# Performance work log

Measured on AMD Instinct MI355X. Metric: run time of the kernel, lower is better.

Reference implementation:

```python
import jax, jax.numpy as jnp
import numpy as np

DIM = 128
HEADS = 4
KV_RANK = 64
Q_RANK = 32
ROPE = DIM // 2   # 64
NOPE = DIM // 2   # 64
VDIM = DIM // 2   # 64
B, H, W = 2, 64, 64
EPS = 1e-5


def _conv1x1(x, w, b):
    # x: [B,C,H,W], w: [O,C], b: [O]
    return jnp.einsum('bchw,oc->bohw', x, w) + b[None, :, None, None]


def _gn1(x, g, b):
    # GroupNorm with 1 group: normalize over (C,H,W) per sample
    mu = jnp.mean(x, axis=(1, 2, 3), keepdims=True)
    var = jnp.mean((x - mu) ** 2, axis=(1, 2, 3), keepdims=True)
    return (x - mu) / jnp.sqrt(var + EPS) * g[None, :, None, None] + b[None, :, None, None]


def _freqs(h, w):
    # Replicates RotaryPositionalEncoding: pe[...,0::4]=sin_h, 1::4=cos_h, 2::4=sin_w, 3::4=cos_w
    n = ROPE // 4
    inv = 1.0 / (10000.0 ** (jnp.arange(n, dtype=jnp.float32) / n))
    ah = jnp.arange(h, dtype=jnp.float32)[:, None] * inv  # [h,n]
    aw = jnp.arange(w, dtype=jnp.float32)[:, None] * inv  # [w,n]
    fh = jnp.stack([jnp.sin(ah), jnp.cos(ah)], -1)  # [h,n,2] -> (real=sin_h, imag=cos_h)
    fw = jnp.stack([jnp.sin(aw), jnp.cos(aw)], -1)  # [w,n,2]
    fh_b = jnp.broadcast_to(fh[:, None], (h, w, n, 2))
    fw_b = jnp.broadcast_to(fw[None, :], (h, w, n, 2))
    # interleave pairs: pair 2m -> fh[m], pair 2m+1 -> fw[m]
    pe = jnp.stack([fh_b, fw_b], axis=3).reshape(h * w, ROPE // 2, 2)
    return pe  # [S, ROPE//2, 2]


def _rope(x, f):
    # x: [..., S, ROPE]; f: [S, ROPE//2, 2]
    xp = x.reshape(x.shape[:-1] + (ROPE // 2, 2))
    fr, fi = f[..., 0], f[..., 1]  # [S, ROPE//2] broadcast over leading dims
    rr = xp[..., 0] * fr - xp[..., 1] * fi
    ri = xp[..., 0] * fi + xp[..., 1] * fr
    return jnp.stack([rr, ri], -1).reshape(x.shape)


def setup_inputs() -> dict:
    key = jax.random.key(0)
    ks = jax.random.split(key, 8)
    s = 0.02
    inp = {
        'x': jax.random.normal(ks[0], (B, DIM, H, W), dtype=jnp.float32),
        'q1_w': jax.random.normal(ks[1], (Q_RANK, DIM), dtype=jnp.float32) * s,
        'q1_b': jnp.zeros((Q_RANK,), jnp.float32),
        'q_gn_g': jnp.ones((Q_RANK,), jnp.float32),
        'q_gn_b': jnp.zeros((Q_RANK,), jnp.float32),
        'q2_w': jax.random.normal(ks[2], (HEADS * (NOPE + ROPE), Q_RANK), dtype=jnp.float32) * s,
        'q2_b': jnp.zeros((HEADS * (NOPE + ROPE),), jnp.float32),
        'kv1_w': jax.random.normal(ks[3], (KV_RANK + ROPE, DIM), dtype=jnp.float32) * s,
        'kv1_b': jnp.zeros((KV_RANK + ROPE,), jnp.float32),
        'kv_gn_g': jnp.ones((KV_RANK + ROPE,), jnp.float32),
        'kv_gn_b': jnp.zeros((KV_RANK + ROPE,), jnp.float32),
        'kvn_g': jnp.ones((KV_RANK,), jnp.float32),
        'kvn_b': jnp.zeros((KV_RANK,), jnp.float32),
        'kvup_w': jax.random.normal(ks[4], (HEADS * (NOPE + VDIM), KV_RANK), dtype=jnp.float32) * s,
        'kvup_b': jnp.zeros((HEADS * (NOPE + VDIM),), jnp.float32),
        'out_w': jax.random.normal(ks[5], (DIM, HEADS * VDIM), dtype=jnp.float32) * s,
        'out_b': jnp.zeros((DIM,), jnp.float32),
    }
    return inp


def reference(x, q1_w, q1_b, q_gn_g, q_gn_b, q2_w, q2_b, kv1_w, kv1_b, kv_gn_g, kv_gn_b, kvn_g, kvn_b, kvup_w, kvup_b, out_w, out_b):
    b, c, h, w = x.shape
    s = h * w
    f = _freqs(h, w)  # [S, ROPE//2, 2]

    # Q path: low-rank down -> GN -> up
    q = _conv1x1(_gn1(_conv1x1(x, q1_w, q1_b), q_gn_g, q_gn_b), q2_w, q2_b)
    q = q.reshape(b, HEADS, NOPE + ROPE, s).transpose(0, 1, 3, 2)  # [B,H,S,D]
    q_nope, q_rope = q[..., :NOPE], q[..., NOPE:]
    q = jnp.concatenate([q_nope, _rope(q_rope, f)], axis=-1)

    # KV path: joint down-proj, split rope-k and compressed kv
    kv = _gn1(_conv1x1(x, kv1_w, kv1_b), kv_gn_g, kv_gn_b)  # [B, ROPE+KV_RANK, H, W]
    k_rope_c, kv_c = kv[:, :ROPE], kv[:, ROPE:]
    kv_u = _conv1x1(_gn1(kv_c, kvn_g, kvn_b), kvup_w, kvup_b)
    kv_u = kv_u.reshape(b, HEADS, NOPE + VDIM, s).transpose(0, 1, 3, 2)
    k_nope, v = kv_u[..., :NOPE], kv_u[..., NOPE:]

    k_rope = _rope(k_rope_c.reshape(b, ROPE, s).transpose(0, 2, 1)[:, None], f)  # [B,1,S,ROPE]
    k = jnp.concatenate([k_nope, jnp.broadcast_to(k_rope, (b, HEADS, s, ROPE))], axis=-1)

    scale = (NOPE + ROPE) ** -0.5
    attn = jax.nn.softmax(jnp.einsum('bhqd,bhkd->bhqk', q, k) * scale, axis=-1)
    o = jnp.einsum('bhqk,bhkd->bhqd', attn, v)  # [B,H,S,VDIM]
    o = o.transpose(0, 1, 3, 2).reshape(b, HEADS * VDIM, h, w)
    return _conv1x1(o, out_w, out_b) + x
```

## Files before the change

kernel.cpp:

```cpp
#include <hip/hip_runtime.h>

typedef unsigned short ushort_t;
typedef unsigned int uint_t;
typedef __attribute__((ext_vector_type(8))) short s16x8;
typedef __attribute__((ext_vector_type(4))) short s16x4;
typedef __attribute__((ext_vector_type(4))) float f32x4;
typedef __attribute__((ext_vector_type(16))) float f32x16;

#define S_TOT 4096
#define QSCALE 0.08838834764831845f
#define LOG2E 1.4426950408889634f
#define QSL (QSCALE * LOG2E)
#define L2_10000_D16 0.8304820237218406f

__device__ __forceinline__ ushort_t f2b(float f) {
  uint_t u = __float_as_uint(f);
  uint_t r = (u + 0x7FFFu + ((u >> 16) & 1u)) >> 16;
  return (ushort_t)r;
}

__device__ __forceinline__ float b2f(ushort_t u) {
  return __uint_as_float((uint_t)u << 16);
}

__device__ __forceinline__ uint_t cvt_pk_bf16(float lo, float hi) {
  uint_t r;
  asm("v_cvt_pk_bf16_f32 %0, %1, %2" : "=v"(r) : "v"(lo), "v"(hi));
  return r;
}

__device__ __forceinline__ void gload16(const void* g, void* l) {
  __builtin_amdgcn_global_load_lds(
      (const __attribute__((address_space(1))) unsigned int*)g,
      (__attribute__((address_space(3))) unsigned int*)l, 16, 0, 0);
}

__device__ __forceinline__ void rope_pair(float& x0, float& x1, int p, int hi, int wi, float scale) {
  float inv = exp2f(-(float)(p >> 1) * L2_10000_D16);
  float ang = ((p & 1) ? (float)wi : (float)hi) * inv;
  float sn = sinf(ang), cs = cosf(ang);
  float r0 = (x0 * sn - x1 * cs) * scale;
  float r1 = (x0 * cs + x1 * sn) * scale;
  x0 = r0; x1 = r1;
}

__global__ __launch_bounds__(256) void k_conv1(
    const float* __restrict__ x, const float* __restrict__ q1_w, const float* __restrict__ q1_b,
    const float* __restrict__ kv1_w, const float* __restrict__ kv1_b,
    float* __restrict__ y_q, float* __restrict__ y_kv, double* __restrict__ pch,
    const float* __restrict__ q2_w, const float* __restrict__ q2_b,
    const float* __restrict__ kvup_w, const float* __restrict__ kvup_b,
    const float* __restrict__ out_w, const float* __restrict__ out_b,
    ushort_t* __restrict__ wq2, ushort_t* __restrict__ wout,
    float* __restrict__ q2b2, float* __restrict__ outb2) {
  if (blockIdx.x >= 512) {
    int E = (blockIdx.x - 512) * 256 + threadIdx.x;
    if (E < 16384) {
      int oc = E >> 5, r = E & 31;
      int h = oc >> 7, d = oc & 127;
      float val;
      if (d < 64) {
        val = 0.f;
        for (int dd = 0; dd < 64; dd++)
          val += kvup_w[(h * 128 + dd) * 64 + d] * q2_w[(size_t)(h * 128 + dd) * 32 + r];
      } else {
        val = q2_w[(size_t)oc * 32 + r];
      }
      wq2[(size_t)oc * 32 + r] = f2b(val);
    } else if (E < 49152) {
      int e = E - 16384;
      int c = e >> 8, col = e & 255;
      int h = col >> 6, l = col & 63;
      float val = 0.f;
      for (int vd = 0; vd < 64; vd++)
        val += out_w[(size_t)c * 256 + h * 64 + vd] * kvup_w[(h * 128 + 64 + vd) * 64 + l];
      wout[(size_t)c * 256 + col] = f2b(val);
    } else if (E < 49664) {
      int oc = E - 49152;
      int h = oc >> 7, d = oc & 127;
      float val;
      if (d < 64) {
        val = 0.f;
        for (int dd = 0; dd < 64; dd++)
          val += kvup_w[(h * 128 + dd) * 64 + d] * q2_b[h * 128 + dd];
      } else val = q2_b[oc];
      q2b2[oc] = val;
    } else if (E < 49792) {
      int c = E - 49664;
      float val = out_b[c];
      for (int j = 0; j < 256; j++) {
        int h = j >> 6, vd = j & 63;
        val += out_w[(size_t)c * 256 + j] * kvup_b[h * 128 + 64 + vd];
      }
      outb2[c] = val;
    }
    return;
  }
  const int b = blockIdx.x >> 8, blk = blockIdx.x & 255, st = blk * 16;
  const int t = threadIdx.x, si = t & 15, g = t >> 4;
  __shared__ float xs[128][16];
#pragma unroll
  for (int i = 0; i < 8; i++) {
    int c = g + 16 * i;
    xs[c][si] = x[(size_t)(b * 128 + c) * S_TOT + st + si];
  }
  __syncthreads();
  float acc[10];
#pragma unroll
  for (int i = 0; i < 10; i++) {
    int oc = g * 10 + i;
    acc[i] = (oc < 32) ? q1_b[oc] : kv1_b[oc - 32];
  }
  const float4* q1w4 = (const float4*)q1_w;
  const float4* kv1w4 = (const float4*)kv1_w;
  for (int c4 = 0; c4 < 32; c4++) {
    float x0 = xs[c4 * 4 + 0][si], x1 = xs[c4 * 4 + 1][si];
    float x2 = xs[c4 * 4 + 2][si], x3 = xs[c4 * 4 + 3][si];
#pragma unroll
    for (int i = 0; i < 10; i++) {
      int oc = g * 10 + i;
      float4 wv = (oc < 32) ? q1w4[oc * 32 + c4] : kv1w4[(oc - 32) * 32 + c4];
      acc[i] += wv.x * x0 + wv.y * x1 + wv.z * x2 + wv.w * x3;
    }
  }
#pragma unroll
  for (int i = 0; i < 10; i++) {
    int oc = g * 10 + i;
    float a = acc[i];
    if (oc < 32) y_q[(size_t)(b * 32 + oc) * S_TOT + st + si] = a;
    else         y_kv[(size_t)(b * 128 + oc - 32) * S_TOT + st + si] = a;
    double s = a, q = (double)a * a;
#pragma unroll
    for (int o = 1; o < 16; o <<= 1) { s += __shfl_xor(s, o, 16); q += __shfl_xor(q, o, 16); }
    if (si == 0) {
      double* pt = pch + (size_t)(b * 160 + oc) * 512 + blk * 2;
      pt[0] = s; pt[1] = q;
    }
  }
}

__global__ __launch_bounds__(256) void k_red(
    const double* __restrict__ pch, double* __restrict__ SQ) {
  const int pair = blockIdx.x, tid = threadIdx.x;
  const int lane = tid & 63, wid = tid >> 6;
  const double* p = pch + (size_t)pair * 512;
  double s = p[tid * 2], q = p[tid * 2 + 1];
#pragma unroll
  for (int o = 1; o < 64; o <<= 1) { s += __shfl_xor(s, o, 64); q += __shfl_xor(q, o, 64); }
  __shared__ double red[4][2];
  if (lane == 0) { red[wid][0] = s; red[wid][1] = q; }
  __syncthreads();
  if (tid == 0) {
    SQ[pair * 2]     = red[0][0] + red[1][0] + red[2][0] + red[3][0];
    SQ[pair * 2 + 1] = red[0][1] + red[1][1] + red[2][1] + red[3][1];
  }
}

__global__ __launch_bounds__(512) void k_stats(
    const double* __restrict__ SQ,
    const float* __restrict__ qg, const float* __restrict__ qb,
    const float* __restrict__ kvg, const float* __restrict__ kvb,
    const float* __restrict__ kng, const float* __restrict__ knb,
    float* __restrict__ coef) {
  __shared__ double Sh[2][160], Qh[2][160];
  const int tid = threadIdx.x;
  if (tid < 320) {
    int b = tid / 160, c = tid % 160;
    Sh[b][c] = SQ[tid * 2]; Qh[b][c] = SQ[tid * 2 + 1];
  }
  __syncthreads();
  if (tid < 2) {
    int b = tid;
    float* cf = coef + b * 320;
    const double NS = 4096.0;
    double muq = 0, m2q = 0;
    for (int c = 0; c < 32; c++) { muq += Sh[b][c]; m2q += Qh[b][c]; }
    muq /= (32.0 * NS); m2q /= (32.0 * NS);
    double rstdq = 1.0 / sqrt(m2q - muq * muq + 1e-5);
    for (int c = 0; c < 32; c++) {
      double A = rstdq * (double)qg[c];
      cf[c] = (float)A; cf[32 + c] = (float)((double)qb[c] - muq * A);
    }
    double mukv = 0, m2kv = 0;
    for (int c = 0; c < 128; c++) { mukv += Sh[b][32 + c]; m2kv += Qh[b][32 + c]; }
    mukv /= (128.0 * NS); m2kv /= (128.0 * NS);
    double rstdkv = 1.0 / sqrt(m2kv - mukv * mukv + 1e-5);
    for (int c = 0; c < 64; c++) {
      double A = rstdkv * (double)kvg[c];
      cf[64 + c] = (float)A; cf[128 + c] = (float)((double)kvb[c] - mukv * A);
    }
    double mu2 = 0, m22 = 0;
    for (int c2 = 0; c2 < 64; c2++) {
      int c = 64 + c2;
      double a = rstdkv * (double)kvg[c], bb = (double)kvb[c] - mukv * a;
      double Ec = Sh[b][32 + c] / NS, M2c = Qh[b][32 + c] / NS;
      mu2 += a * Ec + bb;
      m22 += a * a * M2c + 2.0 * a * bb * Ec + bb * bb;
    }
    mu2 /= 64.0; m22 /= 64.0;
    double rstd2 = 1.0 / sqrt(m22 - mu2 * mu2 + 1e-5);
    for (int c2 = 0; c2 < 64; c2++) {
      int c = 64 + c2;
      double a = rstdkv * (double)kvg[c], bb = (double)kvb[c] - mukv * a;
      cf[192 + c2] = (float)(a * rstd2 * (double)kng[c2]);
      cf[256 + c2] = (float)((bb - mu2) * rstd2 * (double)kng[c2] + (double)knb[c2]);
    }
  }
}

__global__ __launch_bounds__(256) void k_gq(
    const float* __restrict__ y_q, const float* __restrict__ coef,
    const ushort_t* __restrict__ wq2, const float* __restrict__ q2b2,
    ushort_t* __restrict__ Q) {
  const int id = blockIdx.x;
  const int h = id & 3, st = (id >> 2) & 63, b = id >> 8;
  const int t = threadIdx.x, si = t & 63, wid = t >> 6;
  const int l15 = t & 15, lg = (t >> 4) & 3;
  const float* cf = coef + b * 320;
  __shared__ __align__(16) ushort_t Xt[64][64];
  __shared__ __align__(16) ushort_t sQ[64][128];
  {
    ushort_t pk[8];
#pragma unroll
    for (int j = 0; j < 8; j++) {
      int c = wid * 8 + j;
      float v = y_q[(size_t)(b * 32 + c) * S_TOT + st * 64 + si];
      pk[j] = f2b(v * cf[c] + cf[32 + c]);
    }
    *(s16x8*)((char*)&Xt[si][0] + ((wid * 16) ^ ((si & 7) << 4))) = *(s16x8*)pk;
  }
  __syncthreads();
  const int d0w = wid * 32;
  f32x4 acc[2][4];
#pragma unroll
  for (int db = 0; db < 2; db++) {
    f32x4 bv;
#pragma unroll
    for (int r = 0; r < 4; r++) bv[r] = q2b2[h * 128 + d0w + db * 16 + lg * 4 + r];
#pragma unroll
    for (int sb = 0; sb < 4; sb++) acc[db][sb] = bv;
  }
  s16x8 wf[2];
#pragma unroll
  for (int db = 0; db < 2; db++)
    wf[db] = *(const s16x8*)(wq2 + (size_t)(h * 128 + d0w + db * 16 + l15) * 32 + lg * 8);
  const int xsw = (lg * 16) ^ ((l15 & 7) << 4);
#pragma unroll
  for (int sb = 0; sb < 4; sb++) {
    s16x8 xf = *(const s16x8*)((const char*)&Xt[sb * 16 + l15][0] + xsw);
#pragma unroll
    for (int db = 0; db < 2; db++)
      acc[db][sb] = __builtin_amdgcn_mfma_f32_16x16x32_bf16(wf[db], xf, acc[db][sb], 0, 0, 0);
  }
  if (wid >= 2) {
#pragma unroll
    for (int db = 0; db < 2; db++)
#pragma unroll
      for (int sb = 0; sb < 4; sb++) {
        int sp = st * 64 + sb * 16 + l15, hi = sp >> 6, wi = sp & 63;
        int dg = d0w + db * 16 + lg * 4;
#pragma unroll
        for (int pr = 0; pr < 2; pr++) {
          float v0 = acc[db][sb][pr * 2], v1 = acc[db][sb][pr * 2 + 1];
          int p = (dg + pr * 2 - 64) >> 1;
          rope_pair(v0, v1, p, hi, wi, QSL);
          acc[db][sb][pr * 2] = v0; acc[db][sb][pr * 2 + 1] = v1;
        }
      }
  } else {
#pragma unroll
    for (int db = 0; db < 2; db++)
#pragma unroll
      for (int sb = 0; sb < 4; sb++)
#pragma unroll
        for (int r = 0; r < 4; r++) acc[db][sb][r] *= QSL;
  }
#pragma unroll
  for (int db = 0; db < 2; db++)
#pragma unroll
    for (int sb = 0; sb < 4; sb++) {
      ushort_t pk[4];
#pragma unroll
      for (int r = 0; r < 4; r++) pk[r] = f2b(acc[db][sb][r]);
      int srow = sb * 16 + l15;
      *(s16x4*)((char*)&sQ[srow][0] + (((d0w + db * 16 + lg * 4) * 2) ^ ((srow & 7) << 4))) =
          *(s16x4*)pk;
    }
  __syncthreads();
  ushort_t* qrow = Q + ((size_t)(b * 4 + h) * S_TOT + st * 64 + si) * 128 + wid * 32;
#pragma unroll
  for (int j = 0; j < 4; j++) {
    s16x8 v = *(const s16x8*)((const char*)&sQ[si][0] + ((wid * 64 + j * 16) ^ ((si & 7) << 4)));
    *(s16x8*)(qrow + j * 8) = v;
  }
}

__global__ __launch_bounds__(256) void k_lat(
    const float* __restrict__ y_kv, const float* __restrict__ coef,
    ushort_t* __restrict__ C, ushort_t* __restrict__ VT) {
  const int blk = blockIdx.x;
  const int b = blk >> 6, st = (blk & 63) * 64;
  const int t = threadIdx.x, si = t & 63, g = t >> 6;
  const float* cf = coef + b * 320;
  const int sp = st + si;
  if (g < 2) {
    const int c0 = g * 32;
    float v[32];
#pragma unroll
    for (int j = 0; j < 32; j++) {
      int c = c0 + j;
      v[j] = y_kv[(size_t)(b * 128 + c) * S_TOT + sp] * cf[64 + c] + cf[128 + c];
    }
    const int hi = sp >> 6, wi = sp & 63;
#pragma unroll
    for (int k = 0; k < 16; k++)
      rope_pair(v[2 * k], v[2 * k + 1], (c0 >> 1) + k, hi, wi, 1.0f);
    ushort_t pk[32];
#pragma unroll
    for (int j = 0; j < 32; j++) pk[j] = f2b(v[j]);
    ushort_t* crow = C + (size_t)(b * S_TOT + sp) * 128 + 64 + c0;
#pragma unroll
    for (int j4 = 0; j4 < 4; j4++) *(s16x8*)(crow + j4 * 8) = *(s16x8*)(pk + j4 * 8);
  } else {
    const int c0 = (g - 2) * 32;
    ushort_t pk[32];
#pragma unroll
    for (int j = 0; j < 32; j++) {
      int c2 = c0 + j;
      float v = y_kv[(size_t)(b * 128 + 64 + c2) * S_TOT + sp] * cf[192 + c2] + cf[256 + c2];
      ushort_t u = f2b(v);
      pk[j] = u;
      VT[(size_t)(b * 64 + c2) * S_TOT + sp] = u;
    }
    ushort_t* crow = C + (size_t)(b * S_TOT + sp) * 128 + c0;
#pragma unroll
    for (int j4 = 0; j4 < 4; j4++) *(s16x8*)(crow + j4 * 8) = *(s16x8*)(pk + j4 * 8);
  }
}

__global__ __launch_bounds__(256, 2) void k_attn(
    const ushort_t* __restrict__ Q, const ushort_t* __restrict__ C,
    const ushort_t* __restrict__ VT, ushort_t* __restrict__ Opart,
    float* __restrict__ ml) {
  const int bid = blockIdx.x;
  const int bh = bid & 7;
  const int rest = bid >> 3;
  const int half = rest >> 5, qblk = rest & 31;
  const int kv0 = half * 2048;
  const int tid = threadIdx.x;
  const int wid = tid >> 6, lane = tid & 63;
  const int l31 = lane & 31, hi = lane >> 5;
  const int qbase = qblk * 128 + wid * 32;
  const int b4 = bh >> 2;
  const ushort_t* Qp = Q + (size_t)bh * S_TOT * 128;
  const ushort_t* Kp = C + (size_t)b4 * S_TOT * 128;
  const ushort_t* Vp = VT + (size_t)b4 * 64 * S_TOT;

  __shared__ __align__(16) ushort_t K_lds[3][64][128];
  __shared__ __align__(16) ushort_t V_lds[3][64][64];

  s16x8 qf[8];
#pragma unroll
  for (int c = 0; c < 8; c++)
    qf[c] = *(const s16x8*)(Qp + (size_t)(qbase + l31) * 128 + c * 16 + hi * 8);

  f32x16 o0, o1;
#pragma unroll
  for (int r = 0; r < 16; r++) { o0[r] = 0.f; o1[r] = 0.f; }
  float l_s = 0.f;

  const int krow_l = tid >> 4;
  const int kcolb = (tid & 15) * 16;
  const int vrow_l = tid >> 3;
  const int vcolb = (tid & 7) * 16;

#define STAGE(kvb, bufi)                                                          \
  {                                                                               \
    _Pragma("unroll")                                                             \
    for (int i = 0; i < 4; i++) {                                                 \
      int row = i * 16 + krow_l;                                                  \
      int colb = kcolb ^ ((row & 15) << 4);                                       \
      gload16((const char*)(Kp + (size_t)((kvb) + row) * 128) + colb,             \
              (void*)&K_lds[bufi][i * 16 + wid * 4][0]);                          \
    }                                                                             \
    _Pragma("unroll")                                                             \
    for (int i = 0; i < 2; i++) {                                                 \
      int vd = i * 32 + vrow_l;                                                   \
      int colb = vcolb ^ ((vd & 7) << 4);                                         \
      gload16((const char*)(Vp + (size_t)vd * S_TOT + (kvb)) + colb,              \
              (void*)&V_lds[bufi][i * 32 + wid * 8][0]);                          \
    }                                                                             \
  }

  STAGE(kv0, 0);
  STAGE(kv0 + 64, 1);

  const int kswz = (l31 & 15) << 4;
  const int vswz = (l31 & 7) << 4;
#pragma unroll 1
  for (int t = 0; t < 32; t++) {
    const int buf = t % 3;
    if (t < 31) {
      asm volatile("s_waitcnt vmcnt(6)" ::: "memory");
    } else {
      asm volatile("s_waitcnt vmcnt(0)" ::: "memory");
    }
    __builtin_amdgcn_sched_barrier(0);
    __builtin_amdgcn_s_barrier();
    __builtin_amdgcn_sched_barrier(0);
    if (t < 30) STAGE(kv0 + (t + 2) * 64, (t + 2) % 3);
    f32x16 sc0, sc1;
#pragma unroll
    for (int r = 0; r < 16; r++) { sc0[r] = 0.f; sc1[r] = 0.f; }
    __builtin_amdgcn_s_setprio(1);
#pragma unroll
    for (int c = 0; c < 8; c++) {
      const int off = (c * 32 + hi * 16) ^ kswz;
      s16x8 k0 = *(const s16x8*)((const char*)&K_lds[buf][l31][0] + off);
      s16x8 k1 = *(const s16x8*)((const char*)&K_lds[buf][32 + l31][0] + off);
      sc0 = __builtin_amdgcn_mfma_f32_32x32x16_bf16(k0, qf[c], sc0, 0, 0, 0);
      sc1 = __builtin_amdgcn_mfma_f32_32x32x16_bf16(k1, qf[c], sc1, 0, 0, 0);
    }
    __builtin_amdgcn_s_setprio(0);
    float rs = 0.f;
#pragma unroll
    for (int r = 0; r < 16; r++) {
      float p0 = exp2f(sc0[r]);
      float p1 = exp2f(sc1[r]);
      sc0[r] = p0; sc1[r] = p1;
      rs += p0 + p1;
    }
    l_s += rs;
    __builtin_amdgcn_s_setprio(1);
#pragma unroll
    for (int c = 0; c < 4; c++) {
      const f32x16 P = (c < 2) ? sc0 : sc1;
      const int rA = 8 * (c & 1);
      uint_t a0 = cvt_pk_bf16(P[rA + 0], P[rA + 1]);
      uint_t a1 = cvt_pk_bf16(P[rA + 2], P[rA + 3]);
      uint_t b0 = cvt_pk_bf16(P[rA + 4], P[rA + 5]);
      uint_t b1 = cvt_pk_bf16(P[rA + 6], P[rA + 7]);
      asm volatile("v_permlane32_swap_b32 %0, %1" : "+v"(a0), "+v"(b0));
      asm volatile("v_permlane32_swap_b32 %0, %1" : "+v"(a1), "+v"(b1));
      union { uint_t u[4]; s16x8 v; } pf;
      pf.u[0] = a0; pf.u[1] = a1;
      pf.u[2] = b0; pf.u[3] = b1;
      const int voff = (c * 32 + hi * 16) ^ vswz;
      s16x8 v0 = *(const s16x8*)((const char*)&V_lds[buf][l31][0] + voff);
      s16x8 v1 = *(const s16x8*)((const char*)&V_lds[buf][32 + l31][0] + voff);
      o0 = __builtin_amdgcn_mfma_f32_32x32x16_bf16(v0, pf.v, o0, 0, 0, 0);
      o1 = __builtin_amdgcn_mfma_f32_32x32x16_bf16(v1, pf.v, o1, 0, 0, 0);
    }
    __builtin_amdgcn_s_setprio(0);
  }
#undef STAGE
  l_s += __shfl_xor(l_s, 32, 64);
  float linv = 1.f / l_s;
  if (lane < 32) {
    float* mlrow = ml + ((size_t)(half * 8 + bh) * S_TOT + qbase + l31) * 2;
    mlrow[0] = 0.f; mlrow[1] = l_s;
  }
  char* sO = (char*)&K_lds[0][0][0];
#pragma unroll
  for (int vt = 0; vt < 2; vt++) {
#pragma unroll
    for (int r = 0; r < 16; r += 2) {
      float v0 = (vt ? o1[r] : o0[r]) * linv;
      float v1 = (vt ? o1[r + 1] : o0[r + 1]) * linv;
      uint_t u = cvt_pk_bf16(v0, v1);
      int vd = vt * 32 + (r & 3) + 8 * (r >> 2) + 4 * hi;
      *(uint_t*)(sO + (wid * 32 + l31) * 128 + ((vd * 2) ^ ((l31 & 7) << 4))) = u;
    }
  }
  __syncthreads();
  {
    const int r = tid >> 1, hf = tid & 1;
    const int w = r >> 5, ql = r & 31;
    ushort_t* orow = Opart + ((size_t)(half * 8 + bh) * S_TOT + qblk * 128 + r) * 64 + hf * 32;
#pragma unroll
    for (int j = 0; j < 4; j++) {
      s16x8 v = *(const s16x8*)(sO + (w * 32 + ql) * 128 + ((hf * 64 + j * 16) ^ ((ql & 7) << 4)));
      *(s16x8*)(orow + j * 8) = v;
    }
  }
}

__global__ __launch_bounds__(256) void k_oc(
    const ushort_t* __restrict__ Opart, const float* __restrict__ ml,
    const ushort_t* __restrict__ wout, const float* __restrict__ outb2,
    const float* __restrict__ x, float* __restrict__ out) {
  const int id = blockIdx.x;
  const int cch = id & 1, st32 = (id >> 1) & 127, b = id >> 8;
  const int t = threadIdx.x, wid = t >> 6;
  const int l15 = t & 15, lg = (t >> 4) & 3;
  __shared__ __align__(16) ushort_t Xt[32][256];
  {
    const int s = t & 31, grp = t >> 5;
    const int h = grp >> 1, vd0 = (grp & 1) * 32;
    const int sp = st32 * 32 + s;
    const float2 ml0 = *(const float2*)&ml[((size_t)(b * 4 + h) * S_TOT + sp) * 2];
    const float2 ml1 = *(const float2*)&ml[((size_t)(8 + b * 4 + h) * S_TOT + sp) * 2];
    float mm = fmaxf(ml0.x, ml1.x);
    float w0 = exp2f(ml0.x - mm) * ml0.y, w1 = exp2f(ml1.x - mm) * ml1.y;
    float inv = 1.f / (w0 + w1);
    w0 *= inv; w1 *= inv;
    const ushort_t* oa = Opart + ((size_t)(b * 4 + h) * S_TOT + sp) * 64 + vd0;
    const ushort_t* obp = oa + (size_t)8 * S_TOT * 64;
#pragma unroll
    for (int j4 = 0; j4 < 4; j4++) {
      union { s16x8 v; ushort_t u[8]; } av, bv2;
      av.v = *(const s16x8*)(oa + j4 * 8);
      bv2.v = *(const s16x8*)(obp + j4 * 8);
      ushort_t pk[8];
#pragma unroll
      for (int j = 0; j < 8; j++) pk[j] = f2b(w0 * b2f(av.u[j]) + w1 * b2f(bv2.u[j]));
      *(s16x8*)((char*)&Xt[s][0] + ((grp * 64 + j4 * 16) ^ ((s & 7) << 4))) = *(s16x8*)pk;
    }
  }
  __syncthreads();
  const int c0w = cch * 64 + wid * 16;
  f32x4 acc[2];
  {
    f32x4 bv;
#pragma unroll
    for (int r = 0; r < 4; r++) bv[r] = outb2[c0w + lg * 4 + r];
    acc[0] = bv; acc[1] = bv;
  }
#pragma unroll
  for (int kk = 0; kk < 8; kk++) {
    s16x8 wf = *(const s16x8*)(wout + (size_t)(c0w + l15) * 256 + kk * 32 + lg * 8);
#pragma unroll
    for (int sb = 0; sb < 2; sb++) {
      s16x8 xf = *(const s16x8*)((const char*)&Xt[sb * 16 + l15][0] +
                                 ((kk * 64 + lg * 16) ^ ((l15 & 7) << 4)));
      acc[sb] = __builtin_amdgcn_mfma_f32_16x16x32_bf16(wf, xf, acc[sb], 0, 0, 0);
    }
  }
#pragma unroll
  for (int sb = 0; sb < 2; sb++) {
#pragma unroll
    for (int r = 0; r < 4; r++) {
      int c = c0w + lg * 4 + r;
      int sp = st32 * 32 + sb * 16 + l15;
      size_t idx = (size_t)(b * 128 + c) * S_TOT + sp;
      out[idx] = acc[sb][r] + x[idx];
    }
  }
}

extern "C" void kernel_launch(void* const* d_in, const int* in_sizes, int n_in,
                              void* d_out, int out_size, void* d_ws, size_t ws_size,
                              hipStream_t stream) {
  const float* x      = (const float*)d_in[0];
  const float* q1_w   = (const float*)d_in[1];
  const float* q1_b   = (const float*)d_in[2];
  const float* q_gn_g = (const float*)d_in[3];
  const float* q_gn_b = (const float*)d_in[4];
  const float* q2_w   = (const float*)d_in[5];
  const float* q2_b   = (const float*)d_in[6];
  const float* kv1_w  = (const float*)d_in[7];
  const float* kv1_b  = (const float*)d_in[8];
  const float* kv_gn_g= (const float*)d_in[9];
  const float* kv_gn_b= (const float*)d_in[10];
  const float* kvn_g  = (const float*)d_in[11];
  const float* kvn_b  = (const float*)d_in[12];
  const float* kvup_w = (const float*)d_in[13];
  const float* kvup_b = (const float*)d_in[14];
  const float* out_w  = (const float*)d_in[15];
  const float* out_b  = (const float*)d_in[16];

  const size_t MB = 1u << 20;
  char* ws = (char*)d_ws;
  float*    y_q   = (float*)(ws);
  float*    y_kv  = (float*)(ws + 1 * MB);
  ushort_t* Q     = (ushort_t*)(ws + 5 * MB);
  ushort_t* C     = (ushort_t*)(ws + 13 * MB);
  ushort_t* VT    = (ushort_t*)(ws + 15 * MB);
  double*   pch   = (double*)(ws + 17 * MB);
  double*   SQ    = (double*)(ws + 19 * MB);
  float*    coef  = (float*)(ws + 19 * MB + 8192);
  ushort_t* wq2   = (ushort_t*)(ws + 19 * MB + 16384);
  ushort_t* wout  = (ushort_t*)(ws + 19 * MB + 65536);
  float*    q2b2  = (float*)(ws + 19 * MB + 131072);
  float*    outb2 = (float*)(ws + 19 * MB + 139264);
  ushort_t* Opart = (ushort_t*)(ws + 20 * MB);
  float*    ml    = (float*)(ws + 28 * MB);
  float*    out   = (float*)d_out;

  k_conv1<<<707, 256, 0, stream>>>(x, q1_w, q1_b, kv1_w, kv1_b, y_q, y_kv, pch,
                                   q2_w, q2_b, kvup_w, kvup_b, out_w, out_b,
                                   wq2, wout, q2b2, outb2);
  k_red  <<<320, 256, 0, stream>>>(pch, SQ);
  k_stats<<<1,   512, 0, stream>>>(SQ, q_gn_g, q_gn_b, kv_gn_g, kv_gn_b, kvn_g, kvn_b, coef);
  k_gq   <<<512, 256, 0, stream>>>(y_q, coef, wq2, q2b2, Q);
  k_lat  <<<128, 256, 0, stream>>>(y_kv, coef, C, VT);
  k_attn <<<512, 256, 0, stream>>>(Q, C, VT, Opart, ml);
  k_oc   <<<512, 256, 0, stream>>>(Opart, ml, wout, outb2, x, out);
}
```

Measured before the change: 148.2 us.

## Load K/V tiles directly from global into registers instead of LDS staging

```diff
diff --git a/kernel.cpp b/kernel.cpp
--- a/kernel.cpp
+++ b/kernel.cpp
@@ -27,12 +27,6 @@
   uint_t r;
   asm("v_cvt_pk_bf16_f32 %0, %1, %2" : "=v"(r) : "v"(lo), "v"(hi));
   return r;
-}
-
-__device__ __forceinline__ void gload16(const void* g, void* l) {
-  __builtin_amdgcn_global_load_lds(
-      (const __attribute__((address_space(1))) unsigned int*)g,
-      (__attribute__((address_space(3))) unsigned int*)l, 16, 0, 0);
 }
 
 __device__ __forceinline__ void rope_pair(float& x0, float& x1, int p, int hi, int wi, float scale) {
@@ -356,8 +350,7 @@
   const ushort_t* Kp = C + (size_t)b4 * S_TOT * 128;
   const ushort_t* Vp = VT + (size_t)b4 * 64 * S_TOT;
 
-  __shared__ __align__(16) ushort_t K_lds[3][64][128];
-  __shared__ __align__(16) ushort_t V_lds[3][64][64];
+  __shared__ __align__(16) ushort_t sO[4][32][64];
 
   s16x8 qf[8];
 #pragma unroll
@@ -369,98 +362,67 @@
   for (int r = 0; r < 16; r++) { o0[r] = 0.f; o1[r] = 0.f; }
   float l_s = 0.f;
 
-  const int krow_l = tid >> 4;
-  const int kcolb = (tid & 15) * 16;
-  const int vrow_l = tid >> 3;
-  const int vcolb = (tid & 7) * 16;
-
-#define STAGE(kvb, bufi)                                                          \
-  {                                                                               \
-    _Pragma("unroll")                                                             \
-    for (int i = 0; i < 4; i++) {                                                 \
-      int row = i * 16 + krow_l;                                                  \
-      int colb = kcolb ^ ((row & 15) << 4);                                       \
-      gload16((const char*)(Kp + (size_t)((kvb) + row) * 128) + colb,             \
-              (void*)&K_lds[bufi][i * 16 + wid * 4][0]);                          \
-    }                                                                             \
-    _Pragma("unroll")                                                             \
-    for (int i = 0; i < 2; i++) {                                                 \
-      int vd = i * 32 + vrow_l;                                                   \
-      int colb = vcolb ^ ((vd & 7) << 4);                                         \
-      gload16((const char*)(Vp + (size_t)vd * S_TOT + (kvb)) + colb,              \
-              (void*)&V_lds[bufi][i * 32 + wid * 8][0]);                          \
-    }                                                                             \
-  }
-
-  STAGE(kv0, 0);
-  STAGE(kv0 + 64, 1);
-
-  const int kswz = (l31 & 15) << 4;
-  const int vswz = (l31 & 7) << 4;
+  const ushort_t* krow = Kp + (size_t)(kv0 + l31) * 128 + hi * 8;
+  const ushort_t* vrow0 = Vp + (size_t)l31 * S_TOT + kv0 + hi * 8;
+  const ushort_t* vrow1 = Vp + (size_t)(32 + l31) * S_TOT + kv0 + hi * 8;
+
+  s16x8 kc[8], kn[8];
+#pragma unroll
+  for (int c = 0; c < 8; c++) kc[c] = *(const s16x8*)(krow + c * 16);
+
 #pragma unroll 1
-  for (int t = 0; t < 32; t++) {
-    const int buf = t % 3;
-    if (t < 31) {
-      asm volatile("s_waitcnt vmcnt(6)" ::: "memory");
-    } else {
-      asm volatile("s_waitcnt vmcnt(0)" ::: "memory");
-    }
-    __builtin_amdgcn_sched_barrier(0);
-    __builtin_amdgcn_s_barrier();
-    __builtin_amdgcn_sched_barrier(0);
-    if (t < 30) STAGE(kv0 + (t + 2) * 64, (t + 2) % 3);
-    f32x16 sc0, sc1;
-#pragma unroll
-    for (int r = 0; r < 16; r++) { sc0[r] = 0.f; sc1[r] = 0.f; }
+  for (int t = 0; t < 64; t++) {
+    if (t < 63) {
+      const ushort_t* krn = krow + (size_t)(t + 1) * 32 * 128;
+#pragma unroll
+      for (int c = 0; c < 8; c++) kn[c] = *(const s16x8*)(krn + c * 16);
+    }
+    s16x8 va00 = *(const s16x8*)(vrow0 + t * 32);
+    s16x8 va01 = *(const s16x8*)(vrow0 + t * 32 + 16);
+    s16x8 va10 = *(const s16x8*)(vrow1 + t * 32);
+    s16x8 va11 = *(const s16x8*)(vrow1 + t * 32 + 16);
+    f32x16 sc;
+#pragma unroll
+    for (int r = 0; r < 16; r++) sc[r] = 0.f;
     __builtin_amdgcn_s_setprio(1);
 #pragma unroll
-    for (int c = 0; c < 8; c++) {
-      const int off = (c * 32 + hi * 16) ^ kswz;
-      s16x8 k0 = *(const s16x8*)((const char*)&K_lds[buf][l31][0] + off);
-      s16x8 k1 = *(const s16x8*)((const char*)&K_lds[buf][32 + l31][0] + off);
-      sc0 = __builtin_amdgcn_mfma_f32_32x32x16_bf16(k0, qf[c], sc0, 0, 0, 0);
-      sc1 = __builtin_amdgcn_mfma_f32_32x32x16_bf16(k1, qf[c], sc1, 0, 0, 0);
-    }
+    for (int c = 0; c < 8; c++)
+      sc = __builtin_amdgcn_mfma_f32_32x32x16_bf16(kc[c], qf[c], sc, 0, 0, 0);
     __builtin_amdgcn_s_setprio(0);
     float rs = 0.f;
 #pragma unroll
     for (int r = 0; r < 16; r++) {
-      float p0 = exp2f(sc0[r]);
-      float p1 = exp2f(sc1[r]);
-      sc0[r] = p0; sc1[r] = p1;
-      rs += p0 + p1;
+      float p = exp2f(sc[r]);
+      sc[r] = p; rs += p;
     }
     l_s += rs;
     __builtin_amdgcn_s_setprio(1);
 #pragma unroll
-    for (int c = 0; c < 4; c++) {
-      const f32x16 P = (c < 2) ? sc0 : sc1;
-      const int rA = 8 * (c & 1);
-      uint_t a0 = cvt_pk_bf16(P[rA + 0], P[rA + 1]);
-      uint_t a1 = cvt_pk_bf16(P[rA + 2], P[rA + 3]);
-      uint_t b0 = cvt_pk_bf16(P[rA + 4], P[rA + 5]);
-      uint_t b1 = cvt_pk_bf16(P[rA + 6], P[rA + 7]);
+    for (int ks = 0; ks < 2; ks++) {
+      const int rA = 8 * ks;
+      uint_t a0 = cvt_pk_bf16(sc[rA + 0], sc[rA + 1]);
+      uint_t a1 = cvt_pk_bf16(sc[rA + 2], sc[rA + 3]);
+      uint_t b0 = cvt_pk_bf16(sc[rA + 4], sc[rA + 5]);
+      uint_t b1 = cvt_pk_bf16(sc[rA + 6], sc[rA + 7]);
       asm volatile("v_permlane32_swap_b32 %0, %1" : "+v"(a0), "+v"(b0));
       asm volatile("v_permlane32_swap_b32 %0, %1" : "+v"(a1), "+v"(b1));
       union { uint_t u[4]; s16x8 v; } pf;
       pf.u[0] = a0; pf.u[1] = a1;
       pf.u[2] = b0; pf.u[3] = b1;
-      const int voff = (c * 32 + hi * 16) ^ vswz;
-      s16x8 v0 = *(const s16x8*)((const char*)&V_lds[buf][l31][0] + voff);
-      s16x8 v1 = *(const s16x8*)((const char*)&V_lds[buf][32 + l31][0] + voff);
-      o0 = __builtin_amdgcn_mfma_f32_32x32x16_bf16(v0, pf.v, o0, 0, 0, 0);
-      o1 = __builtin_amdgcn_mfma_f32_32x32x16_bf16(v1, pf.v, o1, 0, 0, 0);
+      o0 = __builtin_amdgcn_mfma_f32_32x32x16_bf16(ks ? va01 : va00, pf.v, o0, 0, 0, 0);
+      o1 = __builtin_amdgcn_mfma_f32_32x32x16_bf16(ks ? va11 : va10, pf.v, o1, 0, 0, 0);
     }
     __builtin_amdgcn_s_setprio(0);
-  }
-#undef STAGE
+#pragma unroll
+    for (int c = 0; c < 8; c++) kc[c] = kn[c];
+  }
   l_s += __shfl_xor(l_s, 32, 64);
   float linv = 1.f / l_s;
   if (lane < 32) {
     float* mlrow = ml + ((size_t)(half * 8 + bh) * S_TOT + qbase + l31) * 2;
     mlrow[0] = 0.f; mlrow[1] = l_s;
   }
-  char* sO = (char*)&K_lds[0][0][0];
+  char* sOb = (char*)&sO[0][0][0];
 #pragma unroll
   for (int vt = 0; vt < 2; vt++) {
 #pragma unroll
@@ -469,7 +431,7 @@
       float v1 = (vt ? o1[r + 1] : o0[r + 1]) * linv;
       uint_t u = cvt_pk_bf16(v0, v1);
       int vd = vt * 32 + (r & 3) + 8 * (r >> 2) + 4 * hi;
-      *(uint_t*)(sO + (wid * 32 + l31) * 128 + ((vd * 2) ^ ((l31 & 7) << 4))) = u;
+      *(uint_t*)(sOb + (wid * 32 + l31) * 128 + ((vd * 2) ^ ((l31 & 7) << 4))) = u;
     }
   }
   __syncthreads();
@@ -479,7 +441,7 @@
     ushort_t* orow = Opart + ((size_t)(half * 8 + bh) * S_TOT + qblk * 128 + r) * 64 + hf * 32;
 #pragma unroll
     for (int j = 0; j < 4; j++) {
-      s16x8 v = *(const s16x8*)(sO + (w * 32 + ql) * 128 + ((hf * 64 + j * 16) ^ ((ql & 7) << 4)));
+      s16x8 v = *(const s16x8*)(sOb + (w * 32 + ql) * 128 + ((hf * 64 + j * 16) ^ ((ql & 7) << 4)));
       *(s16x8*)(orow + j * 8) = v;
     }
   }
```

Measured after the change: 250.9 us. +69.3%, slower.

## Merge Q-build and latent-build kernels; pass only row sums to output combine

Applied to the files above, without the earlier changes.

```diff
diff --git a/kernel.cpp b/kernel.cpp
--- a/kernel.cpp
+++ b/kernel.cpp
@@ -208,17 +208,17 @@
   }
 }
 
-__global__ __launch_bounds__(256) void k_gq(
+__device__ __forceinline__ void gq_body(
+    int id, ushort_t* smem,
     const float* __restrict__ y_q, const float* __restrict__ coef,
     const ushort_t* __restrict__ wq2, const float* __restrict__ q2b2,
     ushort_t* __restrict__ Q) {
-  const int id = blockIdx.x;
   const int h = id & 3, st = (id >> 2) & 63, b = id >> 8;
   const int t = threadIdx.x, si = t & 63, wid = t >> 6;
   const int l15 = t & 15, lg = (t >> 4) & 3;
   const float* cf = coef + b * 320;
-  __shared__ __align__(16) ushort_t Xt[64][64];
-  __shared__ __align__(16) ushort_t sQ[64][128];
+  ushort_t* Xt = smem;
+  ushort_t* sQ = smem + 4096;
   {
     ushort_t pk[8];
 #pragma unroll
@@ -227,7 +227,7 @@
       float v = y_q[(size_t)(b * 32 + c) * S_TOT + st * 64 + si];
       pk[j] = f2b(v * cf[c] + cf[32 + c]);
     }
-    *(s16x8*)((char*)&Xt[si][0] + ((wid * 16) ^ ((si & 7) << 4))) = *(s16x8*)pk;
+    *(s16x8*)((char*)(Xt + si * 64) + ((wid * 16) ^ ((si & 7) << 4))) = *(s16x8*)pk;
   }
   __syncthreads();
   const int d0w = wid * 32;
@@ -247,7 +247,7 @@
   const int xsw = (lg * 16) ^ ((l15 & 7) << 4);
 #pragma unroll
   for (int sb = 0; sb < 4; sb++) {
-    s16x8 xf = *(const s16x8*)((const char*)&Xt[sb * 16 + l15][0] + xsw);
+    s16x8 xf = *(const s16x8*)((const char*)(Xt + (sb * 16 + l15) * 64) + xsw);
 #pragma unroll
     for (int db = 0; db < 2; db++)
       acc[db][sb] = __builtin_amdgcn_mfma_f32_16x16x32_bf16(wf[db], xf, acc[db][sb], 0, 0, 0);
@@ -283,22 +283,21 @@
 #pragma unroll
       for (int r = 0; r < 4; r++) pk[r] = f2b(acc[db][sb][r]);
       int srow = sb * 16 + l15;
-      *(s16x4*)((char*)&sQ[srow][0] + (((d0w + db * 16 + lg * 4) * 2) ^ ((srow & 7) << 4))) =
+      *(s16x4*)((char*)(sQ + srow * 128) + (((d0w + db * 16 + lg * 4) * 2) ^ ((srow & 7) << 4))) =
           *(s16x4*)pk;
     }
   __syncthreads();
   ushort_t* qrow = Q + ((size_t)(b * 4 + h) * S_TOT + st * 64 + si) * 128 + wid * 32;
 #pragma unroll
   for (int j = 0; j < 4; j++) {
-    s16x8 v = *(const s16x8*)((const char*)&sQ[si][0] + ((wid * 64 + j * 16) ^ ((si & 7) << 4)));
+    s16x8 v = *(const s16x8*)((const char*)(sQ + si * 128) + ((wid * 64 + j * 16) ^ ((si & 7) << 4)));
     *(s16x8*)(qrow + j * 8) = v;
   }
 }
 
-__global__ __launch_bounds__(256) void k_lat(
-    const float* __restrict__ y_kv, const float* __restrict__ coef,
+__device__ __forceinline__ void lat_body(
+    int blk, const float* __restrict__ y_kv, const float* __restrict__ coef,
     ushort_t* __restrict__ C, ushort_t* __restrict__ VT) {
-  const int blk = blockIdx.x;
   const int b = blk >> 6, st = (blk & 63) * 64;
   const int t = threadIdx.x, si = t & 63, g = t >> 6;
   const float* cf = coef + b * 320;
@@ -338,10 +337,20 @@
   }
 }
 
+__global__ __launch_bounds__(256) void k_build(
+    const float* __restrict__ y_q, const float* __restrict__ y_kv,
+    const float* __restrict__ coef,
+    const ushort_t* __restrict__ wq2, const float* __restrict__ q2b2,
+    ushort_t* __restrict__ Q, ushort_t* __restrict__ C, ushort_t* __restrict__ VT) {
+  __shared__ __align__(16) ushort_t smem[12288];
+  if (blockIdx.x < 512) gq_body(blockIdx.x, smem, y_q, coef, wq2, q2b2, Q);
+  else                  lat_body(blockIdx.x - 512, y_kv, coef, C, VT);
+}
+
 __global__ __launch_bounds__(256, 2) void k_attn(
     const ushort_t* __restrict__ Q, const ushort_t* __restrict__ C,
     const ushort_t* __restrict__ VT, ushort_t* __restrict__ Opart,
-    float* __restrict__ ml) {
+    float* __restrict__ lvec) {
   const int bid = blockIdx.x;
   const int bh = bid & 7;
   const int rest = bid >> 3;
@@ -455,18 +464,15 @@
   }
 #undef STAGE
   l_s += __shfl_xor(l_s, 32, 64);
-  float linv = 1.f / l_s;
-  if (lane < 32) {
-    float* mlrow = ml + ((size_t)(half * 8 + bh) * S_TOT + qbase + l31) * 2;
-    mlrow[0] = 0.f; mlrow[1] = l_s;
-  }
+  if (lane < 32)
+    lvec[((size_t)(half * 8 + bh) << 12) + qbase + l31] = l_s;
   char* sO = (char*)&K_lds[0][0][0];
 #pragma unroll
   for (int vt = 0; vt < 2; vt++) {
 #pragma unroll
     for (int r = 0; r < 16; r += 2) {
-      float v0 = (vt ? o1[r] : o0[r]) * linv;
-      float v1 = (vt ? o1[r + 1] : o0[r + 1]) * linv;
+      float v0 = (vt ? o1[r] : o0[r]);
+      float v1 = (vt ? o1[r + 1] : o0[r + 1]);
       uint_t u = cvt_pk_bf16(v0, v1);
       int vd = vt * 32 + (r & 3) + 8 * (r >> 2) + 4 * hi;
       *(uint_t*)(sO + (wid * 32 + l31) * 128 + ((vd * 2) ^ ((l31 & 7) << 4))) = u;
@@ -486,7 +492,7 @@
 }
 
 __global__ __launch_bounds__(256) void k_oc(
-    const ushort_t* __restrict__ Opart, const float* __restrict__ ml,
+    const ushort_t* __restrict__ Opart, const float* __restrict__ lvec,
     const ushort_t* __restrict__ wout, const float* __restrict__ outb2,
     const float* __restrict__ x, float* __restrict__ out) {
   const int id = blockIdx.x;
@@ -498,12 +504,9 @@
     const int s = t & 31, grp = t >> 5;
     const int h = grp >> 1, vd0 = (grp & 1) * 32;
     const int sp = st32 * 32 + s;
-    const float2 ml0 = *(const float2*)&ml[((size_t)(b * 4 + h) * S_TOT + sp) * 2];
-    const float2 ml1 = *(const float2*)&ml[((size_t)(8 + b * 4 + h) * S_TOT + sp) * 2];
-    float mm = fmaxf(ml0.x, ml1.x);
-    float w0 = exp2f(ml0.x - mm) * ml0.y, w1 = exp2f(ml1.x - mm) * ml1.y;
-    float inv = 1.f / (w0 + w1);
-    w0 *= inv; w1 *= inv;
+    const float l0 = lvec[((size_t)(b * 4 + h) << 12) + sp];
+    const float l1 = lvec[((size_t)(8 + b * 4 + h) << 12) + sp];
+    const float w = 1.f / (l0 + l1);
     const ushort_t* oa = Opart + ((size_t)(b * 4 + h) * S_TOT + sp) * 64 + vd0;
     const ushort_t* obp = oa + (size_t)8 * S_TOT * 64;
 #pragma unroll
@@ -513,7 +516,7 @@
       bv2.v = *(const s16x8*)(obp + j4 * 8);
       ushort_t pk[8];
 #pragma unroll
-      for (int j = 0; j < 8; j++) pk[j] = f2b(w0 * b2f(av.u[j]) + w1 * b2f(bv2.u[j]));
+      for (int j = 0; j < 8; j++) pk[j] = f2b(w * (b2f(av.u[j]) + b2f(bv2.u[j])));
       *(s16x8*)((char*)&Xt[s][0] + ((grp * 64 + j4 * 16) ^ ((s & 7) << 4))) = *(s16x8*)pk;
     }
   }
@@ -584,7 +587,7 @@
   float*    q2b2  = (float*)(ws + 19 * MB + 131072);
   float*    outb2 = (float*)(ws + 19 * MB + 139264);
   ushort_t* Opart = (ushort_t*)(ws + 20 * MB);
-  float*    ml    = (float*)(ws + 28 * MB);
+  float*    lvec  = (float*)(ws + 28 * MB);
   float*    out   = (float*)d_out;
 
   k_conv1<<<707, 256, 0, stream>>>(x, q1_w, q1_b, kv1_w, kv1_b, y_q, y_kv, pch,
@@ -592,8 +595,7 @@
                                    wq2, wout, q2b2, outb2);
   k_red  <<<320, 256, 0, stream>>>(pch, SQ);
   k_stats<<<1,   512, 0, stream>>>(SQ, q_gn_g, q_gn_b, kv_gn_g, kv_gn_b, kvn_g, kvn_b, coef);
-  k_gq   <<<512, 256, 0, stream>>>(y_q, coef, wq2, q2b2, Q);
-  k_lat  <<<128, 256, 0, stream>>>(y_kv, coef, C, VT);
-  k_attn <<<512, 256, 0, stream>>>(Q, C, VT, Opart, ml);
-  k_oc   <<<512, 256, 0, stream>>>(Opart, ml, wout, outb2, x, out);
-}
+  k_build<<<640, 256, 0, stream>>>(y_q, y_kv, coef, wq2, q2b2, Q, C, VT);
+  k_attn <<<512, 256, 0, stream>>>(Q, C, VT, Opart, lvec);
+  k_oc   <<<512, 256, 0, stream>>>(Opart, lvec, wout, outb2, x, out);
+}
```

Measured after the change: 146.3 us. Within noise of the previous version (-1.3%).
